# Kernel optimization log

Hardware: AMD Instinct MI355X
Metric: run time of the kernel (lower is better)

## Reference

```python
import jax, jax.numpy as jnp
import numpy as np

E = 512
H = 8
D = E // H  # head_dims = 64
MAXREL = 512


def setup_inputs() -> dict:
    key = jax.random.key(0)
    ks = jax.random.split(key, 12)
    B, L = 4, 1024
    s_lin = float(np.sqrt(6.0 / (D + D)))  # xavier uniform for (D,D)
    s_fc = float(np.sqrt(6.0 / (E + E)))
    s_tab = float(np.sqrt(6.0 / (2 * MAXREL + 1 + D)))
    return {
        "query": jax.random.normal(ks[0], (B, L, E), jnp.float32),
        "key": jax.random.normal(ks[1], (B, L, E), jnp.float32),
        "value": jax.random.normal(ks[2], (B, L, E), jnp.float32),
        "mask": jax.random.randint(ks[3], (B, 1, 1, L), 0, 2, jnp.int32),
        "Wq": jax.random.uniform(ks[4], (D, D), jnp.float32, -s_lin, s_lin),
        "bq": jnp.zeros((D,), jnp.float32),
        "Wk": jax.random.uniform(ks[5], (D, D), jnp.float32, -s_lin, s_lin),
        "bk": jnp.zeros((D,), jnp.float32),
        "Wv": jax.random.uniform(ks[6], (D, D), jnp.float32, -s_lin, s_lin),
        "bv": jnp.zeros((D,), jnp.float32),
        "Wfc": jax.random.uniform(ks[7], (E, E), jnp.float32, -s_fc, s_fc),
        "bfc": jnp.zeros((E,), jnp.float32),
        "rel_k_table": jax.random.uniform(ks[8], (2 * MAXREL + 1, D), jnp.float32, -s_tab, s_tab),
        "rel_v_table": jax.random.uniform(ks[9], (2 * MAXREL + 1, D), jnp.float32, -s_tab, s_tab),
    }


def _rel_indices(length_q, length_k):
    dist = jnp.arange(length_k)[None, :] - jnp.arange(length_q)[:, None]
    return jnp.clip(dist, -MAXREL, MAXREL) + MAXREL  # [Q, K]


def reference(query, key, value, mask, Wq, bq, Wk, bk, Wv, bv, Wfc, bfc, rel_k_table, rel_v_table):
    B, Q, _ = query.shape
    K = key.shape[1]
    q = query.reshape(B, Q, H, D) @ Wq.T + bq  # per-head linear (same weights all heads)
    k = key.reshape(B, K, H, D) @ Wk.T + bk
    v = value.reshape(B, K, H, D) @ Wv.T + bv

    scores = jnp.einsum("bqhd,bkhd->bhqk", q, k)  # [B,H,Q,K]
    scores = jnp.where(mask == 0, jnp.float32(-1e20), scores)  # mask BEFORE bias & scale, as in source

    idx = _rel_indices(Q, K)
    a_key = rel_k_table[idx]    # [Q,K,D]
    a_val = rel_v_table[idx]    # [Q,K,D]
    scores = scores + jnp.einsum("bqhd,qkd->bhqk", q, a_key)

    attn = jax.nn.softmax(scores / jnp.sqrt(jnp.float32(D)), axis=-1)

    out = jnp.einsum("bhqk,bkhd->bqhd", attn, v)  # standard AV
    out = out + jnp.einsum("bhqk,qkd->bqhd", attn, a_val)  # relative-position value term
    out = out.reshape(B, Q, H * D)
    return out @ Wfc.T + bfc
```

## Files before the change

kernel.cpp:

```cpp
#include <hip/hip_runtime.h>
#include <math.h>

#define BB 4
#define LL 1024
#define EE 512
#define HH 8
#define DD 64
#define MAXREL 512

typedef unsigned short u16;
typedef __attribute__((ext_vector_type(8))) short bf16x8;
typedef __attribute__((ext_vector_type(4))) float f32x4;

__device__ __forceinline__ u16 f2bf(float f) {
    unsigned int u = __float_as_uint(f);
    unsigned int r = (u + 0x7FFFu + ((u >> 16) & 1u)) >> 16;
    return (u16)r;
}
__device__ __forceinline__ float bf2f(u16 b) {
    return __uint_as_float(((unsigned int)b) << 16);
}
__device__ __forceinline__ bf16x8 ldf8_bf(const float* p) {
    const float4 a = *(const float4*)(p);
    const float4 b = *(const float4*)(p + 4);
    bf16x8 r;
    r[0] = (short)f2bf(a.x); r[1] = (short)f2bf(a.y);
    r[2] = (short)f2bf(a.z); r[3] = (short)f2bf(a.w);
    r[4] = (short)f2bf(b.x); r[5] = (short)f2bf(b.y);
    r[6] = (short)f2bf(b.z); r[7] = (short)f2bf(b.w);
    return r;
}

#define MF(A, B, C) __builtin_amdgcn_mfma_f32_16x16x32_bf16((A), (B), (C), 0, 0, 0)
#define EXPSC 0.1803368801111244f

__global__ __launch_bounds__(256) void proj_mfma_kernel(
    const float* __restrict__ q_in, const float* __restrict__ k_in, const float* __restrict__ v_in,
    const float* __restrict__ Wq, const float* __restrict__ bq,
    const float* __restrict__ Wk, const float* __restrict__ bk,
    const float* __restrict__ Wv, const float* __restrict__ bv,
    u16* __restrict__ qb, u16* __restrict__ kb, u16* __restrict__ vtb)
{
    int bh = blockIdx.x; int b = bh >> 3; int h = bh & 7;
    int l0 = blockIdx.y * 64;
    int t = threadIdx.x; int w = t >> 6; int lane = t & 63;
    int lg = lane >> 4, lc = lane & 15;
    int lt = l0 + w * 16;

    bf16x8 wq[4][2], wk[4][2], wv[4][2];
    #pragma unroll
    for (int dt = 0; dt < 4; ++dt)
        #pragma unroll
        for (int kc = 0; kc < 2; ++kc) {
            int d = dt * 16 + lc, ko = kc * 32 + lg * 8;
            wq[dt][kc] = ldf8_bf(Wq + d * DD + ko);
            wk[dt][kc] = ldf8_bf(Wk + d * DD + ko);
            wv[dt][kc] = ldf8_bf(Wv + d * DD + ko);
        }
    size_t xrow = ((size_t)b * LL + lt + lc) * EE + h * DD;
    bf16x8 xq[2], xk[2], xv[2];
    #pragma unroll
    for (int kc = 0; kc < 2; ++kc) {
        int ko = kc * 32 + lg * 8;
        xq[kc] = ldf8_bf(q_in + xrow + ko);
        xk[kc] = ldf8_bf(k_in + xrow + ko);
        xv[kc] = ldf8_bf(v_in + xrow + ko);
    }

    f32x4 aq[4] = {}, ak[4] = {}, av[4] = {};
    #pragma unroll
    for (int dt = 0; dt < 4; ++dt) {
        aq[dt] = MF(wq[dt][0], xq[0], aq[dt]);
        aq[dt] = MF(wq[dt][1], xq[1], aq[dt]);
        ak[dt] = MF(wk[dt][0], xk[0], ak[dt]);
        ak[dt] = MF(wk[dt][1], xk[1], ak[dt]);
        av[dt] = MF(xv[0], wv[dt][0], av[dt]);
        av[dt] = MF(xv[1], wv[dt][1], av[dt]);
    }

    #pragma unroll
    for (int dt = 0; dt < 4; ++dt) {
        u16 tq[4], tk[4], tv[4];
        #pragma unroll
        for (int r = 0; r < 4; ++r) {
            int d = dt * 16 + lg * 4 + r;
            tq[r] = f2bf(aq[dt][r] + bq[d]);
            tk[r] = f2bf(ak[dt][r] + bk[d]);
            tv[r] = f2bf(av[dt][r] + bv[dt * 16 + lc]);
        }
        size_t o = ((size_t)bh * LL + lt + lc) * DD + dt * 16 + lg * 4;
        *(uint2*)&qb[o] = *(uint2*)tq;
        *(uint2*)&kb[o] = *(uint2*)tk;
        size_t ov = ((size_t)bh * DD + dt * 16 + lc) * LL + lt + lg * 4;
        *(uint2*)&vtb[ov] = *(uint2*)tv;
    }
}

__global__ __launch_bounds__(256) void prep_kernel(
    const float* __restrict__ relk, const float* __restrict__ relv, const float* __restrict__ Wfc,
    u16* __restrict__ relk_pad, u16* __restrict__ relvt_pad, u16* __restrict__ wfcb)
{
    int idx = blockIdx.x * 256 + threadIdx.x;
    if (idx < 2048 * DD) {
        int r = idx >> 6, d = idx & 63;
        int j = r - 512; j = j < 0 ? 0 : (j > 2 * MAXREL ? 2 * MAXREL : j);
        relk_pad[idx] = f2bf(relk[j * DD + d]);
        int dd = idx >> 11, c = idx & 2047;
        int j2 = c - 512; j2 = j2 < 0 ? 0 : (j2 > 2 * MAXREL ? 2 * MAXREL : j2);
        relvt_pad[idx] = f2bf(relv[j2 * DD + dd]);
    }
    if (idx < EE * EE) wfcb[idx] = f2bf(Wfc[idx]);
}

__global__ __launch_bounds__(256) void attn_mfma_kernel(
    const u16* __restrict__ qb, const u16* __restrict__ kb, const u16* __restrict__ vtb,
    const int* __restrict__ mask,
    const u16* __restrict__ relk_pad, const u16* __restrict__ relvt_pad,
    u16* __restrict__ attn_out)
{
    __shared__ __align__(16) char smem[57600];
    u16* Vts  = (u16*)(smem + 18432);
    u16* RVts = (u16*)(smem + 27648);
    float* lred = (float*)(smem + 57344);
    float* obuf = (float*)smem;

    int bh = blockIdx.x, b = bh >> 3, h = bh & 7;
    int q0 = blockIdx.y * 32;
    int t = threadIdx.x, lane = t & 63, w = t >> 6;
    int rw = w & 1, cw = w >> 1;
    int rbase = rw * 16, c0a = cw * 32;
    int lg = lane >> 4, lc = lane & 15;
    int ub = c0a - rbase + 16;
    size_t bhL = (size_t)bh * LL;
    const u16* kb_bh = kb + bhL * DD;
    const u16* vt_bh = vtb + (size_t)bh * DD * LL;
    const int* mk_b = mask + b * LL;
    u16* Pw  = (u16*)(smem + 43008) + w * 640;
    u16* Pqw = (u16*)(smem + 48128) + w * 1152;

    int sr0 = t >> 3, ss0 = (t & 7) * 8;
    int sr1 = sr0 + 32;
    int rv_row = t >> 2, rv_q = (t & 3) * 24;
    const u16* rvg = relvt_pad + (size_t)rv_row * 2048 + rv_q;
    u16* rvl = RVts + rv_row * 120 + rv_q;
    const u16* rk_base = relk_pad + (size_t)(ub + lc) * DD + lg * 8;

    const u16* qrow = qb + (bhL + q0 + rbase + lc) * DD;
    bf16x8 qf0 = *(const bf16x8*)&qrow[lg * 8];
    bf16x8 qf1 = *(const bf16x8*)&qrow[32 + lg * 8];

    f32x4 s0, s1, g0, g1, g2;
    bf16x8 rk0, rk1, rk2, rk3, rk4, rk5;
    f32x4 oacc[4] = {};
    float lacc[4] = {0.f, 0.f, 0.f, 0.f};
    int delta0 = lc - lg * 4;

#define LOAD_RK(SB) do { \
    const u16* rkp_ = rk_base + (size_t)(SB) * DD; \
    rk0 = *(const bf16x8*)&rkp_[0]; \
    rk1 = *(const bf16x8*)&rkp_[32]; \
    rk2 = *(const bf16x8*)&rkp_[16 * DD]; \
    rk3 = *(const bf16x8*)&rkp_[16 * DD + 32]; \
    rk4 = *(const bf16x8*)&rkp_[32 * DD]; \
    rk5 = *(const bf16x8*)&rkp_[32 * DD + 32]; \
} while (0)

#define DO_SCORES(KBASE) do { \
    const u16* kp0_ = (KBASE) + (c0a + lc) * 72; \
    const u16* kp1_ = (KBASE) + (c0a + 16 + lc) * 72; \
    s0 = (f32x4){0.f,0.f,0.f,0.f}; s1 = s0; g0 = s0; g1 = s0; g2 = s0; \
    __builtin_amdgcn_s_setprio(1); \
    s0 = MF(qf0, *(const bf16x8*)&kp0_[lg * 8], s0); \
    s0 = MF(qf1, *(const bf16x8*)&kp0_[32 + lg * 8], s0); \
    s1 = MF(qf0, *(const bf16x8*)&kp1_[lg * 8], s1); \
    s1 = MF(qf1, *(const bf16x8*)&kp1_[32 + lg * 8], s1); \
    g0 = MF(qf0, rk0, g0); g0 = MF(qf1, rk1, g0); \
    g1 = MF(qf0, rk2, g1); g1 = MF(qf1, rk3, g1); \
    g2 = MF(qf0, rk4, g2); g2 = MF(qf1, rk5, g2); \
    __builtin_amdgcn_s_setprio(0); \
} while (0)

#define DO_SOFTMAX(MB0, MB1) do { \
    _Pragma("unroll") \
    for (int r = 0; r < 4; ++r) { \
        int d_ = delta0 - r; \
        int src_ = (lane & 48) | (d_ & 15); \
        float a0_ = __shfl(g0[r], src_, 64); \
        float a1_ = __shfl(g1[r], src_, 64); \
        float a2_ = __shfl(g2[r], src_, 64); \
        float gv0_ = (d_ >= 0) ? a1_ : a0_; \
        float gv1_ = (d_ >= 0) ? a2_ : a1_; \
        float p0_ = exp2f((s0[r] + (MB0) + gv0_) * EXPSC); \
        float p1_ = exp2f((s1[r] + (MB1) + gv1_) * EXPSC); \
        u16 pb0_ = f2bf(p0_), pb1_ = f2bf(p1_); \
        lacc[r] += p0_ + p1_; \
        int row_ = lg * 4 + r; \
        Pw[row_ * 40 + lc] = pb0_; \
        Pw[row_ * 40 + 16 + lc] = pb1_; \
        Pqw[row_ * 72 + lc - row_ + 16] = pb0_; \
        Pqw[row_ * 72 + 32 + lc - row_] = pb1_; \
    } \
} while (0)

    #pragma unroll
    for (int i = 0; i < 3; ++i) {
        int u = lane + i * 64;
        if (u < 144) *(uint4*)&Pqw[u * 8] = make_uint4(0, 0, 0, 0);
    }
    if (t < 192) {
        int row = t / 3, j = t - row * 3;
        *(uint4*)&RVts[row * 120 + 96 + j * 8] = make_uint4(0, 0, 0, 0);
    }
    int sb0 = 992 - q0;
    {
        u16* Ks0 = (u16*)smem;
        u16* Ks1 = (u16*)(smem + 9216);
        *(uint4*)&Ks0[sr0 * 72 + ss0] = *(const uint4*)&kb_bh[(size_t)sr0 * DD + ss0];
        *(uint4*)&Ks0[sr1 * 72 + ss0] = *(const uint4*)&kb_bh[(size_t)sr1 * DD + ss0];
        *(uint4*)&Ks1[sr0 * 72 + ss0] = *(const uint4*)&kb_bh[(size_t)(64 + sr0) * DD + ss0];
        *(uint4*)&Ks1[sr1 * 72 + ss0] = *(const uint4*)&kb_bh[(size_t)(64 + sr1) * DD + ss0];
        *(uint4*)&Vts[sr0 * 72 + ss0] = *(const uint4*)&vt_bh[(size_t)sr0 * LL + ss0];
        *(uint4*)&Vts[sr1 * 72 + ss0] = *(const uint4*)&vt_bh[(size_t)sr1 * LL + ss0];
        *(uint4*)&rvl[0]  = *(const uint4*)&rvg[sb0];
        *(uint4*)&rvl[8]  = *(const uint4*)&rvg[sb0 + 8];
        *(uint4*)&rvl[16] = *(const uint4*)&rvg[sb0 + 16];
    }
    LOAD_RK(sb0);
    float mbp0 = (mk_b[c0a + lc] != 0) ? 0.f : -1e20f;
    float mbp1 = (mk_b[c0a + 16 + lc] != 0) ? 0.f : -1e20f;
    __syncthreads();
    DO_SCORES((const u16*)smem);
    LOAD_RK(sb0 + 64);
    DO_SOFTMAX(mbp0, mbp1);

    #pragma unroll 1
    for (int c = 0; c < 16; ++c) {
        int k0 = c * 64;
        int sb_ = k0 - q0 + 992;
        uint4 rK0, rK1, rV0, rV1;
        float mbn0 = 0.f, mbn1 = 0.f;
        if (c < 14) {
            rK0 = *(const uint4*)&kb_bh[(size_t)(k0 + 128 + sr0) * DD + ss0];
            rK1 = *(const uint4*)&kb_bh[(size_t)(k0 + 128 + sr1) * DD + ss0];
        }
        if (c < 15) {
            int k0n = k0 + 64;
            rV0 = *(const uint4*)&vt_bh[(size_t)sr0 * LL + k0n + ss0];
            rV1 = *(const uint4*)&vt_bh[(size_t)sr1 * LL + k0n + ss0];
            mbn0 = (mk_b[k0n + c0a + lc] != 0) ? 0.f : -1e20f;
            mbn1 = (mk_b[k0n + c0a + 16 + lc] != 0) ? 0.f : -1e20f;
        }

        bf16x8 pa  = *(const bf16x8*)&Pw[lc * 40 + lg * 8];
        bf16x8 pq0 = *(const bf16x8*)&Pqw[lc * 72 + lg * 8];
        bf16x8 pq1 = *(const bf16x8*)&Pqw[lc * 72 + 32 + lg * 8];

        if (c < 15) {
            const u16* kcur = (const u16*)(smem + ((c + 1) & 1) * 9216);
            DO_SCORES(kcur);
            if (c < 14) LOAD_RK(sb_ + 128);
        }

        __builtin_amdgcn_s_setprio(1);
        #pragma unroll
        for (int dt = 0; dt < 4; ++dt) {
            const u16* vp = &Vts[(dt * 16 + lc) * 72 + c0a];
            const u16* rp = &RVts[(dt * 16 + lc) * 120 + ub];
            oacc[dt] = MF(pa,  *(const bf16x8*)&vp[lg * 8], oacc[dt]);
            oacc[dt] = MF(pq0, *(const bf16x8*)&rp[lg * 8], oacc[dt]);
            oacc[dt] = MF(pq1, *(const bf16x8*)&rp[32 + lg * 8], oacc[dt]);
        }
        __builtin_amdgcn_s_setprio(0);

        if (c < 15) {
            DO_SOFTMAX(mbn0, mbn1);
            int sbn = sb_ + 64;
            uint4 bb0 = *(const uint4*)&rvg[sbn];
            uint4 bb1 = *(const uint4*)&rvg[sbn + 8];
            uint4 bb2 = *(const uint4*)&rvg[sbn + 16];
            __syncthreads();
            if (c < 14) {
                u16* kwr = (u16*)(smem + (c & 1) * 9216);
                *(uint4*)&kwr[sr0 * 72 + ss0] = rK0;
                *(uint4*)&kwr[sr1 * 72 + ss0] = rK1;
            }
            *(uint4*)&Vts[sr0 * 72 + ss0] = rV0;
            *(uint4*)&Vts[sr1 * 72 + ss0] = rV1;
            *(uint4*)&rvl[0]  = bb0;
            *(uint4*)&rvl[8]  = bb1;
            *(uint4*)&rvl[16] = bb2;
            __syncthreads();
        }
    }
#undef LOAD_RK
#undef DO_SCORES
#undef DO_SOFTMAX

    #pragma unroll
    for (int m2 = 1; m2 <= 8; m2 <<= 1) {
        #pragma unroll
        for (int r = 0; r < 4; ++r) lacc[r] += __shfl_xor(lacc[r], m2);
    }
    __syncthreads();
    if (lc == 0) {
        #pragma unroll
        for (int r = 0; r < 4; ++r) lred[cw * 32 + rbase + lg * 4 + r] = lacc[r];
    }
    __syncthreads();
    if (cw == 1) {
        #pragma unroll
        for (int dt = 0; dt < 4; ++dt)
            #pragma unroll
            for (int r = 0; r < 4; ++r)
                obuf[(rbase + lg * 4 + r) * 68 + dt * 16 + lc] = oacc[dt][r];
    }
    __syncthreads();
    if (cw == 0) {
        float inv[4];
        #pragma unroll
        for (int r = 0; r < 4; ++r) {
            int row = rbase + lg * 4 + r;
            inv[r] = 1.0f / (lred[row] + lred[32 + row]);
        }
        #pragma unroll
        for (int dt = 0; dt < 4; ++dt) {
            #pragma unroll
            for (int r = 0; r < 4; ++r) {
                int row = rbase + lg * 4 + r;
                float v = (oacc[dt][r] + obuf[row * 68 + dt * 16 + lc]) * inv[r];
                attn_out[((size_t)b * LL + q0 + row) * EE + h * DD + dt * 16 + lc] = f2bf(v);
            }
        }
    }
}

__global__ __launch_bounds__(256) void fc_mfma_kernel(
    const u16* __restrict__ Xb, const u16* __restrict__ Wb,
    const float* __restrict__ bfc, float* __restrict__ out)
{
    __shared__ u16 As[128][72];
    __shared__ u16 Bs[128][72];
    int m0 = blockIdx.x * 128, n0 = blockIdx.y * 128;
    int t = threadIdx.x, lane = t & 63, w = t >> 6;
    int rw = w & 1, cw = w >> 1;
    int lg = lane >> 4, lc = lane & 15;
    f32x4 acc[4][4] = {};

    for (int kt = 0; kt < EE; kt += 64) {
        __syncthreads();
        #pragma unroll
        for (int i = 0; i < 4; ++i) {
            int unit = i * 256 + t;
            int row = unit >> 3, s = unit & 7;
            *(uint4*)&As[row][s * 8] = *(const uint4*)&Xb[(size_t)(m0 + row) * EE + kt + s * 8];
            *(uint4*)&Bs[row][s * 8] = *(const uint4*)&Wb[(size_t)(n0 + row) * EE + kt + s * 8];
        }
        __syncthreads();
        #pragma unroll
        for (int kc = 0; kc < 2; ++kc) {
            bf16x8 af[4], bf[4];
            #pragma unroll
            for (int i = 0; i < 4; ++i) {
                af[i] = *(const bf16x8*)&As[rw * 64 + i * 16 + lc][kc * 32 + lg * 8];
                bf[i] = *(const bf16x8*)&Bs[cw * 64 + i * 16 + lc][kc * 32 + lg * 8];
            }
            #pragma unroll
            for (int mi = 0; mi < 4; ++mi)
                #pragma unroll
                for (int ni = 0; ni < 4; ++ni)
                    acc[mi][ni] = MF(af[mi], bf[ni], acc[mi][ni]);
        }
    }
    #pragma unroll
    for (int mi = 0; mi < 4; ++mi) {
        #pragma unroll
        for (int ni = 0; ni < 4; ++ni) {
            int n = n0 + cw * 64 + ni * 16 + lc;
            float bias = bfc[n];
            #pragma unroll
            for (int r = 0; r < 4; ++r) {
                int m = m0 + rw * 64 + mi * 16 + lg * 4 + r;
                out[(size_t)m * EE + n] = acc[mi][ni][r] + bias;
            }
        }
    }
}

extern "C" void kernel_launch(void* const* d_in, const int* in_sizes, int n_in,
                              void* d_out, int out_size, void* d_ws, size_t ws_size,
                              hipStream_t stream) {
    const float* query = (const float*)d_in[0];
    const float* key   = (const float*)d_in[1];
    const float* value = (const float*)d_in[2];
    const int*   mask  = (const int*)d_in[3];
    const float* Wq  = (const float*)d_in[4];
    const float* bq  = (const float*)d_in[5];
    const float* Wk  = (const float*)d_in[6];
    const float* bk  = (const float*)d_in[7];
    const float* Wv  = (const float*)d_in[8];
    const float* bv  = (const float*)d_in[9];
    const float* Wfc = (const float*)d_in[10];
    const float* bfc = (const float*)d_in[11];
    const float* relk = (const float*)d_in[12];
    const float* relv = (const float*)d_in[13];
    float* out = (float*)d_out;

    char* ws = (char*)d_ws;
    u16* qb        = (u16*)(ws);
    u16* kb        = (u16*)(ws + (4u << 20));
    u16* vtb       = (u16*)(ws + (8u << 20));
    u16* attnb     = (u16*)(ws + (12u << 20));
    u16* relk_pad  = (u16*)(ws + (16u << 20));
    u16* relvt_pad = (u16*)(ws + (16u << 20) + 262144);
    u16* wfcb      = (u16*)(ws + (16u << 20) + 524288);

    proj_mfma_kernel<<<dim3(BB * HH, LL / 64), 256, 0, stream>>>(
        query, key, value, Wq, bq, Wk, bk, Wv, bv, qb, kb, vtb);
    prep_kernel<<<1024, 256, 0, stream>>>(relk, relv, Wfc, relk_pad, relvt_pad, wfcb);
    attn_mfma_kernel<<<dim3(BB * HH, LL / 32), 256, 0, stream>>>(
        qb, kb, vtb, mask, relk_pad, relvt_pad, attnb);
    fc_mfma_kernel<<<dim3(BB * LL / 128, EE / 128), 256, 0, stream>>>(attnb, wfcb, bfc, out);
}
```

Baseline: 109.5 us.

## Process 64 query rows per attention block with 512 threads sharing K/V tiles

The attention kernel now handles 64 query rows per block using 8 waves instead of 32 rows with 4 waves, so each K, V and relative-V tile staged in shared memory serves twice as many queries. The per-thread global-to-shared copy work is halved and the relative-V window is widened to cover the larger query range. This cuts redundant global/L2 traffic for K/V at the cost of more LDS per block (about 76KB), fewer blocks, and possibly lower occupancy.

```diff
diff --git a/kernel.cpp b/kernel.cpp
--- a/kernel.cpp
+++ b/kernel.cpp
@@ -112,38 +112,37 @@
     if (idx < EE * EE) wfcb[idx] = f2bf(Wfc[idx]);
 }
 
-__global__ __launch_bounds__(256) void attn_mfma_kernel(
+__global__ __launch_bounds__(512) void attn_mfma_kernel(
     const u16* __restrict__ qb, const u16* __restrict__ kb, const u16* __restrict__ vtb,
     const int* __restrict__ mask,
     const u16* __restrict__ relk_pad, const u16* __restrict__ relvt_pad,
     u16* __restrict__ attn_out)
 {
-    __shared__ __align__(16) char smem[57600];
+    __shared__ __align__(16) char smem[76288];
     u16* Vts  = (u16*)(smem + 18432);
     u16* RVts = (u16*)(smem + 27648);
-    float* lred = (float*)(smem + 57344);
+    float* lred = (float*)(smem + 75776);
     float* obuf = (float*)smem;
 
     int bh = blockIdx.x, b = bh >> 3, h = bh & 7;
-    int q0 = blockIdx.y * 32;
+    int q0 = blockIdx.y * 64;
     int t = threadIdx.x, lane = t & 63, w = t >> 6;
-    int rw = w & 1, cw = w >> 1;
-    int rbase = rw * 16, c0a = cw * 32;
+    int qh = w >> 2, cw = (w >> 1) & 1, rw = w & 1;
+    int rbase = qh * 32 + rw * 16, c0a = cw * 32;
     int lg = lane >> 4, lc = lane & 15;
-    int ub = c0a - rbase + 16;
+    int ub_k = c0a - rbase + 16;
+    int ub_v = c0a - rbase + 48;
     size_t bhL = (size_t)bh * LL;
     const u16* kb_bh = kb + bhL * DD;
     const u16* vt_bh = vtb + (size_t)bh * DD * LL;
     const int* mk_b = mask + b * LL;
-    u16* Pw  = (u16*)(smem + 43008) + w * 640;
-    u16* Pqw = (u16*)(smem + 48128) + w * 1152;
-
-    int sr0 = t >> 3, ss0 = (t & 7) * 8;
-    int sr1 = sr0 + 32;
-    int rv_row = t >> 2, rv_q = (t & 3) * 24;
+    u16* Pw  = (u16*)(smem + 47104) + w * 640;
+    u16* Pqw = (u16*)(smem + 57344) + w * 1152;
+
+    int sr = t >> 3, ss = (t & 7) * 8;
+    int rv_row = t >> 3, rv_q = (t & 7) * 16;
     const u16* rvg = relvt_pad + (size_t)rv_row * 2048 + rv_q;
-    u16* rvl = RVts + rv_row * 120 + rv_q;
-    const u16* rk_base = relk_pad + (size_t)(ub + lc) * DD + lg * 8;
+    u16* rvl = RVts + rv_row * 152 + rv_q;
 
     const u16* qrow = qb + (bhL + q0 + rbase + lc) * DD;
     bf16x8 qf0 = *(const bf16x8*)&qrow[lg * 8];
@@ -156,7 +155,7 @@
     int delta0 = lc - lg * 4;
 
 #define LOAD_RK(SB) do { \
-    const u16* rkp_ = rk_base + (size_t)(SB) * DD; \
+    const u16* rkp_ = relk_pad + (size_t)((SB) + ub_k + lc) * DD + lg * 8; \
     rk0 = *(const bf16x8*)&rkp_[0]; \
     rk1 = *(const bf16x8*)&rkp_[32]; \
     rk2 = *(const bf16x8*)&rkp_[16 * DD]; \
@@ -209,21 +208,18 @@
     }
     if (t < 192) {
         int row = t / 3, j = t - row * 3;
-        *(uint4*)&RVts[row * 120 + 96 + j * 8] = make_uint4(0, 0, 0, 0);
+        *(uint4*)&RVts[row * 152 + 128 + j * 8] = make_uint4(0, 0, 0, 0);
     }
     int sb0 = 992 - q0;
+    int sv0 = 960 - q0;
     {
         u16* Ks0 = (u16*)smem;
         u16* Ks1 = (u16*)(smem + 9216);
-        *(uint4*)&Ks0[sr0 * 72 + ss0] = *(const uint4*)&kb_bh[(size_t)sr0 * DD + ss0];
-        *(uint4*)&Ks0[sr1 * 72 + ss0] = *(const uint4*)&kb_bh[(size_t)sr1 * DD + ss0];
-        *(uint4*)&Ks1[sr0 * 72 + ss0] = *(const uint4*)&kb_bh[(size_t)(64 + sr0) * DD + ss0];
-        *(uint4*)&Ks1[sr1 * 72 + ss0] = *(const uint4*)&kb_bh[(size_t)(64 + sr1) * DD + ss0];
-        *(uint4*)&Vts[sr0 * 72 + ss0] = *(const uint4*)&vt_bh[(size_t)sr0 * LL + ss0];
-        *(uint4*)&Vts[sr1 * 72 + ss0] = *(const uint4*)&vt_bh[(size_t)sr1 * LL + ss0];
-        *(uint4*)&rvl[0]  = *(const uint4*)&rvg[sb0];
-        *(uint4*)&rvl[8]  = *(const uint4*)&rvg[sb0 + 8];
-        *(uint4*)&rvl[16] = *(const uint4*)&rvg[sb0 + 16];
+        *(uint4*)&Ks0[sr * 72 + ss] = *(const uint4*)&kb_bh[(size_t)sr * DD + ss];
+        *(uint4*)&Ks1[sr * 72 + ss] = *(const uint4*)&kb_bh[(size_t)(64 + sr) * DD + ss];
+        *(uint4*)&Vts[sr * 72 + ss] = *(const uint4*)&vt_bh[(size_t)sr * LL + ss];
+        *(uint4*)&rvl[0] = *(const uint4*)&rvg[sv0];
+        *(uint4*)&rvl[8] = *(const uint4*)&rvg[sv0 + 8];
     }
     LOAD_RK(sb0);
     float mbp0 = (mk_b[c0a + lc] != 0) ? 0.f : -1e20f;
@@ -237,16 +233,16 @@
     for (int c = 0; c < 16; ++c) {
         int k0 = c * 64;
         int sb_ = k0 - q0 + 992;
-        uint4 rK0, rK1, rV0, rV1;
+        uint4 rK0, rV0, rRV0, rRV1;
         float mbn0 = 0.f, mbn1 = 0.f;
-        if (c < 14) {
-            rK0 = *(const uint4*)&kb_bh[(size_t)(k0 + 128 + sr0) * DD + ss0];
-            rK1 = *(const uint4*)&kb_bh[(size_t)(k0 + 128 + sr1) * DD + ss0];
-        }
+        if (c < 14)
+            rK0 = *(const uint4*)&kb_bh[(size_t)(k0 + 128 + sr) * DD + ss];
         if (c < 15) {
             int k0n = k0 + 64;
-            rV0 = *(const uint4*)&vt_bh[(size_t)sr0 * LL + k0n + ss0];
-            rV1 = *(const uint4*)&vt_bh[(size_t)sr1 * LL + k0n + ss0];
+            int svn = k0n - q0 + 960;
+            rV0  = *(const uint4*)&vt_bh[(size_t)sr * LL + k0n + ss];
+            rRV0 = *(const uint4*)&rvg[svn];
+            rRV1 = *(const uint4*)&rvg[svn + 8];
             mbn0 = (mk_b[k0n + c0a + lc] != 0) ? 0.f : -1e20f;
             mbn1 = (mk_b[k0n + c0a + 16 + lc] != 0) ? 0.f : -1e20f;
         }
@@ -265,7 +261,7 @@
         #pragma unroll
         for (int dt = 0; dt < 4; ++dt) {
             const u16* vp = &Vts[(dt * 16 + lc) * 72 + c0a];
-            const u16* rp = &RVts[(dt * 16 + lc) * 120 + ub];
+            const u16* rp = &RVts[(dt * 16 + lc) * 152 + ub_v];
             oacc[dt] = MF(pa,  *(const bf16x8*)&vp[lg * 8], oacc[dt]);
             oacc[dt] = MF(pq0, *(const bf16x8*)&rp[lg * 8], oacc[dt]);
             oacc[dt] = MF(pq1, *(const bf16x8*)&rp[32 + lg * 8], oacc[dt]);
@@ -274,21 +270,14 @@
 
         if (c < 15) {
             DO_SOFTMAX(mbn0, mbn1);
-            int sbn = sb_ + 64;
-            uint4 bb0 = *(const uint4*)&rvg[sbn];
-            uint4 bb1 = *(const uint4*)&rvg[sbn + 8];
-            uint4 bb2 = *(const uint4*)&rvg[sbn + 16];
             __syncthreads();
             if (c < 14) {
                 u16* kwr = (u16*)(smem + (c & 1) * 9216);
-                *(uint4*)&kwr[sr0 * 72 + ss0] = rK0;
-                *(uint4*)&kwr[sr1 * 72 + ss0] = rK1;
+                *(uint4*)&kwr[sr * 72 + ss] = rK0;
             }
-            *(uint4*)&Vts[sr0 * 72 + ss0] = rV0;
-            *(uint4*)&Vts[sr1 * 72 + ss0] = rV1;
-            *(uint4*)&rvl[0]  = bb0;
-            *(uint4*)&rvl[8]  = bb1;
-            *(uint4*)&rvl[16] = bb2;
+            *(uint4*)&Vts[sr * 72 + ss] = rV0;
+            *(uint4*)&rvl[0] = rRV0;
+            *(uint4*)&rvl[8] = rRV1;
             __syncthreads();
         }
     }
@@ -304,7 +293,7 @@
     __syncthreads();
     if (lc == 0) {
         #pragma unroll
-        for (int r = 0; r < 4; ++r) lred[cw * 32 + rbase + lg * 4 + r] = lacc[r];
+        for (int r = 0; r < 4; ++r) lred[cw * 64 + rbase + lg * 4 + r] = lacc[r];
     }
     __syncthreads();
     if (cw == 1) {
@@ -320,7 +309,7 @@
         #pragma unroll
         for (int r = 0; r < 4; ++r) {
             int row = rbase + lg * 4 + r;
-            inv[r] = 1.0f / (lred[row] + lred[32 + row]);
+            inv[r] = 1.0f / (lred[row] + lred[64 + row]);
         }
         #pragma unroll
         for (int dt = 0; dt < 4; ++dt) {
@@ -417,7 +406,7 @@
     proj_mfma_kernel<<<dim3(BB * HH, LL / 64), 256, 0, stream>>>(
         query, key, value, Wq, bq, Wk, bk, Wv, bv, qb, kb, vtb);
     prep_kernel<<<1024, 256, 0, stream>>>(relk, relv, Wfc, relk_pad, relvt_pad, wfcb);
-    attn_mfma_kernel<<<dim3(BB * HH, LL / 32), 256, 0, stream>>>(
+    attn_mfma_kernel<<<dim3(BB * HH, LL / 64), 512, 0, stream>>>(
         qb, kb, vtb, mask, relk_pad, relvt_pad, attnb);
     fc_mfma_kernel<<<dim3(BB * LL / 128, EE / 128), 256, 0, stream>>>(attnb, wfcb, bfc, out);
 }
```

Result: no change. 109.9 us (+0.3%).

## Read rel-V fragments from global directly, single-buffer K to shrink LDS

Applied to the files above, without the earlier changes.

The attention kernel no longer stages the relative-position value table through shared memory. Each wave now loads its rel-V MFMA operands straight from global memory (an L2-resident table), and the K tile drops from double to single buffering with an extra sync-guarded prologue load. This cuts LDS from about 57.6KB to 33KB per block, which should allow more blocks per CU. It also replaces the software bf16 rounding of the two probabilities with a packed v_cvt_pk_bf16_f32 instruction. The cost is more global loads per iteration and VGPR pressure from eight extra fragments, and there is less overlap on the K tile.

```diff
diff --git a/kernel.cpp b/kernel.cpp
--- a/kernel.cpp
+++ b/kernel.cpp
@@ -16,9 +16,6 @@
     unsigned int u = __float_as_uint(f);
     unsigned int r = (u + 0x7FFFu + ((u >> 16) & 1u)) >> 16;
     return (u16)r;
-}
-__device__ __forceinline__ float bf2f(u16 b) {
-    return __uint_as_float(((unsigned int)b) << 16);
 }
 __device__ __forceinline__ bf16x8 ldf8_bf(const float* p) {
     const float4 a = *(const float4*)(p);
@@ -118,10 +115,10 @@
     const u16* __restrict__ relk_pad, const u16* __restrict__ relvt_pad,
     u16* __restrict__ attn_out)
 {
-    __shared__ __align__(16) char smem[57600];
-    u16* Vts  = (u16*)(smem + 18432);
-    u16* RVts = (u16*)(smem + 27648);
-    float* lred = (float*)(smem + 57344);
+    __shared__ __align__(16) char smem[33024];
+    u16* Ks   = (u16*)(smem);
+    u16* Vts  = (u16*)(smem + 9216);
+    float* lred = (float*)(smem + 32768);
     float* obuf = (float*)smem;
 
     int bh = blockIdx.x, b = bh >> 3, h = bh & 7;
@@ -135,15 +132,13 @@
     const u16* kb_bh = kb + bhL * DD;
     const u16* vt_bh = vtb + (size_t)bh * DD * LL;
     const int* mk_b = mask + b * LL;
-    u16* Pw  = (u16*)(smem + 43008) + w * 640;
-    u16* Pqw = (u16*)(smem + 48128) + w * 1152;
+    u16* Pw  = (u16*)(smem + 18432) + w * 640;
+    u16* Pqw = (u16*)(smem + 23552) + w * 1152;
 
     int sr0 = t >> 3, ss0 = (t & 7) * 8;
     int sr1 = sr0 + 32;
-    int rv_row = t >> 2, rv_q = (t & 3) * 24;
-    const u16* rvg = relvt_pad + (size_t)rv_row * 2048 + rv_q;
-    u16* rvl = RVts + rv_row * 120 + rv_q;
     const u16* rk_base = relk_pad + (size_t)(ub + lc) * DD + lg * 8;
+    const u16* rv_base = relvt_pad + (size_t)lc * 2048 + ub + lg * 8;
 
     const u16* qrow = qb + (bhL + q0 + rbase + lc) * DD;
     bf16x8 qf0 = *(const bf16x8*)&qrow[lg * 8];
@@ -165,9 +160,9 @@
     rk5 = *(const bf16x8*)&rkp_[32 * DD + 32]; \
 } while (0)
 
-#define DO_SCORES(KBASE) do { \
-    const u16* kp0_ = (KBASE) + (c0a + lc) * 72; \
-    const u16* kp1_ = (KBASE) + (c0a + 16 + lc) * 72; \
+#define DO_SCORES() do { \
+    const u16* kp0_ = Ks + (c0a + lc) * 72; \
+    const u16* kp1_ = Ks + (c0a + 16 + lc) * 72; \
     s0 = (f32x4){0.f,0.f,0.f,0.f}; s1 = s0; g0 = s0; g1 = s0; g2 = s0; \
     __builtin_amdgcn_s_setprio(1); \
     s0 = MF(qf0, *(const bf16x8*)&kp0_[lg * 8], s0); \
@@ -192,7 +187,9 @@
         float gv1_ = (d_ >= 0) ? a2_ : a1_; \
         float p0_ = exp2f((s0[r] + (MB0) + gv0_) * EXPSC); \
         float p1_ = exp2f((s1[r] + (MB1) + gv1_) * EXPSC); \
-        u16 pb0_ = f2bf(p0_), pb1_ = f2bf(p1_); \
+        unsigned pk_; \
+        asm("v_cvt_pk_bf16_f32 %0, %1, %2" : "=v"(pk_) : "v"(p0_), "v"(p1_)); \
+        u16 pb0_ = (u16)pk_, pb1_ = (u16)(pk_ >> 16); \
         lacc[r] += p0_ + p1_; \
         int row_ = lg * 4 + r; \
         Pw[row_ * 40 + lc] = pb0_; \
@@ -207,36 +204,45 @@
         int u = lane + i * 64;
         if (u < 144) *(uint4*)&Pqw[u * 8] = make_uint4(0, 0, 0, 0);
     }
-    if (t < 192) {
-        int row = t / 3, j = t - row * 3;
-        *(uint4*)&RVts[row * 120 + 96 + j * 8] = make_uint4(0, 0, 0, 0);
-    }
     int sb0 = 992 - q0;
-    {
-        u16* Ks0 = (u16*)smem;
-        u16* Ks1 = (u16*)(smem + 9216);
-        *(uint4*)&Ks0[sr0 * 72 + ss0] = *(const uint4*)&kb_bh[(size_t)sr0 * DD + ss0];
-        *(uint4*)&Ks0[sr1 * 72 + ss0] = *(const uint4*)&kb_bh[(size_t)sr1 * DD + ss0];
-        *(uint4*)&Ks1[sr0 * 72 + ss0] = *(const uint4*)&kb_bh[(size_t)(64 + sr0) * DD + ss0];
-        *(uint4*)&Ks1[sr1 * 72 + ss0] = *(const uint4*)&kb_bh[(size_t)(64 + sr1) * DD + ss0];
-        *(uint4*)&Vts[sr0 * 72 + ss0] = *(const uint4*)&vt_bh[(size_t)sr0 * LL + ss0];
-        *(uint4*)&Vts[sr1 * 72 + ss0] = *(const uint4*)&vt_bh[(size_t)sr1 * LL + ss0];
-        *(uint4*)&rvl[0]  = *(const uint4*)&rvg[sb0];
-        *(uint4*)&rvl[8]  = *(const uint4*)&rvg[sb0 + 8];
-        *(uint4*)&rvl[16] = *(const uint4*)&rvg[sb0 + 16];
-    }
+    *(uint4*)&Ks[sr0 * 72 + ss0] = *(const uint4*)&kb_bh[(size_t)sr0 * DD + ss0];
+    *(uint4*)&Ks[sr1 * 72 + ss0] = *(const uint4*)&kb_bh[(size_t)sr1 * DD + ss0];
+    *(uint4*)&Vts[sr0 * 72 + ss0] = *(const uint4*)&vt_bh[(size_t)sr0 * LL + ss0];
+    *(uint4*)&Vts[sr1 * 72 + ss0] = *(const uint4*)&vt_bh[(size_t)sr1 * LL + ss0];
     LOAD_RK(sb0);
     float mbp0 = (mk_b[c0a + lc] != 0) ? 0.f : -1e20f;
     float mbp1 = (mk_b[c0a + 16 + lc] != 0) ? 0.f : -1e20f;
     __syncthreads();
-    DO_SCORES((const u16*)smem);
+    DO_SCORES();
     LOAD_RK(sb0 + 64);
     DO_SOFTMAX(mbp0, mbp1);
+    {
+        uint4 k1a = *(const uint4*)&kb_bh[(size_t)(64 + sr0) * DD + ss0];
+        uint4 k1b = *(const uint4*)&kb_bh[(size_t)(64 + sr1) * DD + ss0];
+        __syncthreads();
+        *(uint4*)&Ks[sr0 * 72 + ss0] = k1a;
+        *(uint4*)&Ks[sr1 * 72 + ss0] = k1b;
+        __syncthreads();
+    }
 
     #pragma unroll 1
     for (int c = 0; c < 16; ++c) {
         int k0 = c * 64;
         int sb_ = k0 - q0 + 992;
+
+        const u16* rvp0 = rv_base + sb_;
+        const u16* rvp1 = rvp0 + 16 * 2048;
+        const u16* rvp2 = rvp0 + 32 * 2048;
+        const u16* rvp3 = rvp0 + 48 * 2048;
+        bf16x8 rv00 = *(const bf16x8*)(rvp0);
+        bf16x8 rv01 = *(const bf16x8*)(rvp0 + 32);
+        bf16x8 rv10 = *(const bf16x8*)(rvp1);
+        bf16x8 rv11 = *(const bf16x8*)(rvp1 + 32);
+        bf16x8 rv20 = *(const bf16x8*)(rvp2);
+        bf16x8 rv21 = *(const bf16x8*)(rvp2 + 32);
+        bf16x8 rv30 = *(const bf16x8*)(rvp3);
+        bf16x8 rv31 = *(const bf16x8*)(rvp3 + 32);
+
         uint4 rK0, rK1, rV0, rV1;
         float mbn0 = 0.f, mbn1 = 0.f;
         if (c < 14) {
@@ -256,8 +262,7 @@
         bf16x8 pq1 = *(const bf16x8*)&Pqw[lc * 72 + 32 + lg * 8];
 
         if (c < 15) {
-            const u16* kcur = (const u16*)(smem + ((c + 1) & 1) * 9216);
-            DO_SCORES(kcur);
+            DO_SCORES();
             if (c < 14) LOAD_RK(sb_ + 128);
         }
 
@@ -265,30 +270,23 @@
         #pragma unroll
         for (int dt = 0; dt < 4; ++dt) {
             const u16* vp = &Vts[(dt * 16 + lc) * 72 + c0a];
-            const u16* rp = &RVts[(dt * 16 + lc) * 120 + ub];
-            oacc[dt] = MF(pa,  *(const bf16x8*)&vp[lg * 8], oacc[dt]);
-            oacc[dt] = MF(pq0, *(const bf16x8*)&rp[lg * 8], oacc[dt]);
-            oacc[dt] = MF(pq1, *(const bf16x8*)&rp[32 + lg * 8], oacc[dt]);
-        }
+            oacc[dt] = MF(pa, *(const bf16x8*)&vp[lg * 8], oacc[dt]);
+        }
+        oacc[0] = MF(pq0, rv00, oacc[0]); oacc[0] = MF(pq1, rv01, oacc[0]);
+        oacc[1] = MF(pq0, rv10, oacc[1]); oacc[1] = MF(pq1, rv11, oacc[1]);
+        oacc[2] = MF(pq0, rv20, oacc[2]); oacc[2] = MF(pq1, rv21, oacc[2]);
+        oacc[3] = MF(pq0, rv30, oacc[3]); oacc[3] = MF(pq1, rv31, oacc[3]);
         __builtin_amdgcn_s_setprio(0);
 
         if (c < 15) {
             DO_SOFTMAX(mbn0, mbn1);
-            int sbn = sb_ + 64;
-            uint4 bb0 = *(const uint4*)&rvg[sbn];
-            uint4 bb1 = *(const uint4*)&rvg[sbn + 8];
-            uint4 bb2 = *(const uint4*)&rvg[sbn + 16];
             __syncthreads();
             if (c < 14) {
-                u16* kwr = (u16*)(smem + (c & 1) * 9216);
-                *(uint4*)&kwr[sr0 * 72 + ss0] = rK0;
-                *(uint4*)&kwr[sr1 * 72 + ss0] = rK1;
+                *(uint4*)&Ks[sr0 * 72 + ss0] = rK0;
+                *(uint4*)&Ks[sr1 * 72 + ss0] = rK1;
             }
             *(uint4*)&Vts[sr0 * 72 + ss0] = rV0;
             *(uint4*)&Vts[sr1 * 72 + ss0] = rV1;
-            *(uint4*)&rvl[0]  = bb0;
-            *(uint4*)&rvl[8]  = bb1;
-            *(uint4*)&rvl[16] = bb2;
             __syncthreads();
         }
     }
```

After: 153.0 us. +39.7%, slower.
